# Optimization experiments

Measured on AMD Instinct MI355X. Metric: run time of the kernel, lower is better.

The kernel has to match this reference:

```python
import jax, jax.numpy as jnp
import numpy as np

V, E = 32000, 256
B, S = 8, 512
NA, NC, NS = 12, 24, 576  # N_AXIOMS, N_COMPOSITES, N_STATE
DECAY = 0.9
EPS = 1e-5


def _xavier(key, shape):
    fan_in, fan_out = shape[0], shape[1]
    lim = np.sqrt(6.0 / (fan_in + fan_out))
    return jax.random.uniform(key, shape, jnp.float32, -lim, lim)


def setup_inputs() -> dict:
    key = jax.random.key(0)
    ks = jax.random.split(key, 8)
    return {
        "input_ids": jax.random.randint(ks[0], (B, S), 0, V),
        "embed_table": 0.02 * jax.random.normal(ks[1], (V, E), jnp.float32),
        "ax_w": _xavier(ks[2], (E, NA)), "ax_b": jnp.zeros((NA,), jnp.float32),
        "ax_g": jnp.ones((NA,), jnp.float32), "ax_beta": jnp.zeros((NA,), jnp.float32),
        "comp_w": _xavier(ks[3], (NA, NC)), "comp_b": jnp.zeros((NC,), jnp.float32),
        "comp_g": jnp.ones((NC,), jnp.float32), "comp_beta": jnp.zeros((NC,), jnp.float32),
        "mix": jnp.asarray(0.1, jnp.float32),
        "out_w1": _xavier(ks[4], (NS, 512)), "out_b1": jnp.zeros((512,), jnp.float32),
        "out_w2": _xavier(ks[5], (512, V)), "out_b2": jnp.zeros((V,), jnp.float32),
    }


def _ln(x, g, b):
    m = jnp.mean(x, axis=-1, keepdims=True)
    v = jnp.var(x, axis=-1, keepdims=True)
    return (x - m) * jax.lax.rsqrt(v + EPS) * g + b


def reference(input_ids, embed_table, ax_w, ax_b, ax_g, ax_beta,
              comp_w, comp_b, comp_g, comp_beta, mix,
              out_w1, out_b1, out_w2, out_b2):
    # Embedding lookup (dropout is identity at eval)
    embeds = embed_table[input_ids]                              # [B,S,E]
    # The axiom/composite branches have no time dependence -> compute all steps at once
    axioms = jnp.tanh(_ln(embeds @ ax_w + ax_b, ax_g, ax_beta))  # [B,S,12]
    comps = jnp.tanh(_ln(axioms @ comp_w + comp_b, comp_g, comp_beta))  # [B,S,24]

    sig_mix = jax.nn.sigmoid(mix)
    state0 = jnp.zeros((input_ids.shape[0], NC, NC), jnp.float32)

    def step(state, c):  # c: [B,24]
        state = DECAY * state + sig_mix * (c[:, :, None] * c[:, None, :])
        h = jax.nn.gelu(state.reshape(state.shape[0], NS) @ out_w1 + out_b1,
                        approximate=False)
        logits = h @ out_w2 + out_b2                             # [B,V]
        return state, logits

    final_state, logits = jax.lax.scan(step, state0, jnp.swapaxes(comps, 0, 1))
    return jnp.swapaxes(logits, 0, 1), final_state               # [B,S,V], [B,24,24]
```

## Files before the change

kernel.cpp:

```cpp
#include <hip/hip_runtime.h>
#include <hip/hip_bf16.h>
#include <math.h>

#define BB 8
#define SS 512
#define VV 32000
#define EE 256
#define NAx 12
#define NCc 24
#define NSt 576
#define MM (BB*SS)

typedef __bf16 bf16x8 __attribute__((ext_vector_type(8)));
typedef float f32x4 __attribute__((ext_vector_type(4)));

#define MFMA16(a, b, c) __builtin_amdgcn_mfma_f32_16x16x32_bf16((a), (b), (c), 0, 0, 0)

__device__ __forceinline__ void gl2lds16(const void* g, void* l) {
  __builtin_amdgcn_global_load_lds(
      (const __attribute__((address_space(1))) void*)g,
      (__attribute__((address_space(3))) void*)l, 16, 0, 0);
}

#define FENCE() asm volatile("" ::: "memory")
#define BAR()   do { FENCE(); __builtin_amdgcn_s_barrier(); FENCE(); } while (0)

__global__ __launch_bounds__(256) void k_transpose64(
    const float* __restrict__ in, __hip_bfloat16* __restrict__ out, int R, int C)
{
  __shared__ float t[64][65];
  const int tx = threadIdx.x, ty = threadIdx.y;
  const int c0 = blockIdx.x * 64, r0 = blockIdx.y * 64;
#pragma unroll
  for (int i = 0; i < 64; i += 4)
    t[ty + i][tx] = in[(size_t)(r0 + ty + i) * C + (c0 + tx)];
  __syncthreads();
#pragma unroll
  for (int i = 0; i < 64; i += 4)
    out[(size_t)(c0 + ty + i) * R + (r0 + tx)] = __float2bfloat16(t[tx][ty + i]);
}

__global__ __launch_bounds__(64) void k_embed_comps(
    const int* __restrict__ ids, const float* __restrict__ ET,
    const float* __restrict__ axw, const float* __restrict__ axb,
    const float* __restrict__ axg, const float* __restrict__ axbeta,
    const float* __restrict__ cw,  const float* __restrict__ cb,
    const float* __restrict__ cg,  const float* __restrict__ cbeta,
    float* __restrict__ comps)
{
  __shared__ float sw[EE * NAx];
  __shared__ float scw[NAx * NCc];
  const int tid = threadIdx.x;
  for (int i = tid; i < EE * NAx; i += 64) sw[i] = axw[i];
  for (int i = tid; i < NAx * NCc; i += 64) scw[i] = cw[i];
  __syncthreads();

  const int m = blockIdx.x * 64 + tid;
  const int id = ids[m];
  const float4* e4 = reinterpret_cast<const float4*>(ET + (size_t)id * EE);

  float a[NAx];
#pragma unroll
  for (int t = 0; t < NAx; ++t) a[t] = axb[t];

  for (int q = 0; q < EE / 4; ++q) {
    float4 v = e4[q];
#pragma unroll
    for (int c = 0; c < 4; ++c) {
      float x = (c == 0) ? v.x : (c == 1) ? v.y : (c == 2) ? v.z : v.w;
      const float* wrow = &sw[(q * 4 + c) * NAx];
#pragma unroll
      for (int t = 0; t < NAx; ++t) a[t] += x * wrow[t];
    }
  }
  {
    float mean = 0.f;
#pragma unroll
    for (int t = 0; t < NAx; ++t) mean += a[t];
    mean *= (1.0f / NAx);
    float var = 0.f;
#pragma unroll
    for (int t = 0; t < NAx; ++t) { float d = a[t] - mean; var += d * d; }
    var *= (1.0f / NAx);
    float rs = rsqrtf(var + 1e-5f);
#pragma unroll
    for (int t = 0; t < NAx; ++t)
      a[t] = tanhf((a[t] - mean) * rs * axg[t] + axbeta[t]);
  }
  float c24[NCc];
#pragma unroll
  for (int j = 0; j < NCc; ++j) c24[j] = cb[j];
#pragma unroll
  for (int t = 0; t < NAx; ++t) {
    float x = a[t];
    const float* wrow = &scw[t * NCc];
#pragma unroll
    for (int j = 0; j < NCc; ++j) c24[j] += x * wrow[j];
  }
  {
    float mean = 0.f;
#pragma unroll
    for (int j = 0; j < NCc; ++j) mean += c24[j];
    mean *= (1.0f / NCc);
    float var = 0.f;
#pragma unroll
    for (int j = 0; j < NCc; ++j) { float d = c24[j] - mean; var += d * d; }
    var *= (1.0f / NCc);
    float rs = rsqrtf(var + 1e-5f);
#pragma unroll
    for (int j = 0; j < NCc; ++j)
      c24[j] = tanhf((c24[j] - mean) * rs * cg[j] + cbeta[j]);
  }
#pragma unroll
  for (int j = 0; j < NCc; ++j) comps[(size_t)m * NCc + j] = c24[j];
}

__global__ __launch_bounds__(576) void k_recurrence(
    const float* __restrict__ comps, const float* __restrict__ mix,
    __hip_bfloat16* __restrict__ ST, float* __restrict__ fstate)
{
  __shared__ float sc[SS * NCc];
  const int b = blockIdx.x, tid = threadIdx.x;
  const float* src = comps + (size_t)b * SS * NCc;
  for (int i = tid; i < SS * NCc; i += 576) sc[i] = src[i];
  __syncthreads();

  const float sm = 1.0f / (1.0f + expf(-mix[0]));
  const int i = tid / NCc, j = tid - i * NCc;
  float st = 0.0f;
  __hip_bfloat16* stp = ST + (size_t)b * SS * NSt + tid;
  for (int t = 0; t < SS; ++t) {
    float ci = sc[t * NCc + i], cj = sc[t * NCc + j];
    st = 0.9f * st + sm * ci * cj;
    stp[(size_t)t * NSt] = __float2bfloat16(st);
  }
  fstate[b * NSt + tid] = st;
}

__global__ __launch_bounds__(256) void k_gemm_bt_gelu(
    const __hip_bfloat16* __restrict__ A,
    const __hip_bfloat16* __restrict__ Bt,
    const float* __restrict__ bias,
    __hip_bfloat16* __restrict__ Cb,
    int M, int N, int K)
{
  __shared__ __align__(16) __hip_bfloat16 As[128 * 32];
  __shared__ __align__(16) __hip_bfloat16 Bs[128 * 32];
  const int tid  = threadIdx.x;
  const int lane = tid & 63;
  const int w    = tid >> 6;
  const int wr   = w >> 1, wc = w & 1;
  const int m0 = blockIdx.y * 128;
  const int n0 = blockIdx.x * 128;
  const int lr = lane & 15;
  const int kb = lane >> 4;

  f32x4 acc[4][4];
#pragma unroll
  for (int i = 0; i < 4; ++i)
#pragma unroll
    for (int j = 0; j < 4; ++j) acc[i][j] = (f32x4){0.f, 0.f, 0.f, 0.f};

  for (int k0 = 0; k0 < K; k0 += 32) {
    __syncthreads();
#pragma unroll
    for (int p = 0; p < 2; ++p) {
      const int lbase = w * 2048 + p * 1024;
      const int o  = lbase + lane * 16;
      const int r  = o >> 6;
      const int sg = (o >> 4) & 3;
      gl2lds16(A  + (size_t)(m0 + r) * K + k0 + sg * 8, (char*)As + lbase);
      gl2lds16(Bt + (size_t)(n0 + r) * K + k0 + sg * 8, (char*)Bs + lbase);
    }
    asm volatile("s_waitcnt vmcnt(0)" ::: "memory");
    __syncthreads();

    bf16x8 af[4], bv[4];
#pragma unroll
    for (int mr = 0; mr < 4; ++mr)
      af[mr] = *reinterpret_cast<const bf16x8*>(&As[(wr * 64 + mr * 16 + lr) * 32 + kb * 8]);
#pragma unroll
    for (int nr = 0; nr < 4; ++nr)
      bv[nr] = *reinterpret_cast<const bf16x8*>(&Bs[(wc * 64 + nr * 16 + lr) * 32 + kb * 8]);
#pragma unroll
    for (int mr = 0; mr < 4; ++mr)
#pragma unroll
      for (int nr = 0; nr < 4; ++nr)
        acc[mr][nr] = MFMA16(af[mr], bv[nr], acc[mr][nr]);
  }

#pragma unroll
  for (int nr = 0; nr < 4; ++nr) {
    const int col = n0 + wc * 64 + nr * 16 + lr;
    const float bvs = bias[col];
#pragma unroll
    for (int mr = 0; mr < 4; ++mr) {
      const int rbase = m0 + wr * 64 + mr * 16 + kb * 4;
#pragma unroll
      for (int r = 0; r < 4; ++r) {
        float v = acc[mr][nr][r] + bvs;
        v = 0.5f * v * (1.0f + erff(v * 0.70710678118654752f));
        Cb[(size_t)(rbase + r) * N + col] = __float2bfloat16(v);
      }
    }
  }
}

__global__ __launch_bounds__(256, 2) void k_gemm2_128(
    const __hip_bfloat16* __restrict__ A,
    const __hip_bfloat16* __restrict__ Bt,
    const float* __restrict__ bias,
    float* __restrict__ C,
    int M, int N, int K, int tiles_m)
{
  __shared__ __align__(16) char smem[65536];

  const int NK  = K >> 6;
  const int tid = threadIdx.x;
  const int lane = tid & 63;
  const int w  = tid >> 6;
  const int wr = w >> 1;
  const int wc = w & 1;
  const int lr = lane & 15;
  const int kb = lane >> 4;

  const int nwg = gridDim.x;
  const int cpx = nwg >> 3;
  const int s   = ((int)blockIdx.x & 7) * cpx + ((int)blockIdx.x >> 3);
  const int nt  = s / tiles_m;
  const int mt  = s - nt * tiles_m;
  const int m0  = mt << 7;
  const int n0  = nt << 7;

  const int srow = tid >> 3;
  const int scol = ((tid & 7) ^ (srow & 7)) << 3;
  const int swz0 = (kb ^ (lr & 7)) << 4;
  const int swz1 = swz0 ^ 64;

#define STAGE_A(buf, R, tk0)                                              \
  gl2lds16(A + (size_t)(m0 + (R) + srow) * K + (tk0) + scol,              \
           smem + (buf)*16384 + (R)*128 + w*1024)
#define STAGE_B(buf, R, tk0)                                              \
  gl2lds16(Bt + (size_t)(n0 + (R) + srow) * K + (tk0) + scol,             \
           smem + 32768 + (buf)*16384 + (R)*128 + w*1024)

#define LDA(buf, mf, kh) \
  (*(const bf16x8*)(smem + (buf)*16384 + (wr*64 + (mf)*16 + lr)*128 + ((kh) ? swz1 : swz0)))
#define LDB(buf, nf, kh) \
  (*(const bf16x8*)(smem + 32768 + (buf)*16384 + (wc*64 + (nf)*16 + lr)*128 + ((kh) ? swz1 : swz0)))

  f32x4 acc[4][4];
#pragma unroll
  for (int i = 0; i < 4; ++i)
#pragma unroll
    for (int j = 0; j < 4; ++j) acc[i][j] = (f32x4){0.f, 0.f, 0.f, 0.f};

  float bvs[4];
#pragma unroll
  for (int nf = 0; nf < 4; ++nf) bvs[nf] = bias[n0 + wc * 64 + nf * 16 + lr];

  STAGE_A(0, 0, 0);  STAGE_A(0, 32, 0);  STAGE_A(0, 64, 0);  STAGE_A(0, 96, 0);
  STAGE_B(0, 0, 0);  STAGE_B(0, 32, 0);  STAGE_B(0, 64, 0);  STAGE_B(0, 96, 0);
  STAGE_B(1, 0, 64); STAGE_B(1, 32, 64); STAGE_B(1, 64, 64); STAGE_B(1, 96, 64);
  asm volatile("s_waitcnt vmcnt(4)" ::: "memory");
  BAR();

#pragma unroll 1
  for (int t = 0; t < NK; ++t) {
    const int c  = t & 1;
    const int k1 = (t + 1) << 6;
    const int k2 = (t + 2) << 6;
    bf16x8 a0[4], b0[4], a1[4], b1[4];

#pragma unroll
    for (int mf = 0; mf < 4; ++mf) a0[mf] = LDA(c, mf, 0);
#pragma unroll
    for (int nf = 0; nf < 4; ++nf) b0[nf] = LDB(c, nf, 0);
    if (t < NK - 1) { STAGE_A(c ^ 1, 0, k1); STAGE_A(c ^ 1, 32, k1); }
    BAR();
    asm volatile("s_waitcnt lgkmcnt(0)" ::: "memory");
    __builtin_amdgcn_sched_barrier(0);
    __builtin_amdgcn_s_setprio(1);
#pragma unroll
    for (int mf = 0; mf < 4; ++mf) {
      acc[mf][0] = MFMA16(a0[mf], b0[0], acc[mf][0]);
      acc[mf][1] = MFMA16(a0[mf], b0[1], acc[mf][1]);
    }
    __builtin_amdgcn_s_setprio(0);
    BAR();

#pragma unroll
    for (int mf = 0; mf < 4; ++mf) a1[mf] = LDA(c, mf, 1);
#pragma unroll
    for (int nf = 0; nf < 4; ++nf) b1[nf] = LDB(c, nf, 1);
    if (t < NK - 1) { STAGE_A(c ^ 1, 64, k1); STAGE_A(c ^ 1, 96, k1); }
    BAR();
    asm volatile("s_waitcnt lgkmcnt(0)" ::: "memory");
    __builtin_amdgcn_sched_barrier(0);
    __builtin_amdgcn_s_setprio(1);
#pragma unroll
    for (int mf = 0; mf < 4; ++mf) {
      acc[mf][2] = MFMA16(a0[mf], b0[2], acc[mf][2]);
      acc[mf][3] = MFMA16(a0[mf], b0[3], acc[mf][3]);
    }
    __builtin_amdgcn_s_setprio(0);
    BAR();

    if (t < NK - 2) { STAGE_B(c, 0, k2); STAGE_B(c, 32, k2); }
    BAR();
    __builtin_amdgcn_s_setprio(1);
#pragma unroll
    for (int mf = 0; mf < 4; ++mf) {
      acc[mf][0] = MFMA16(a1[mf], b1[0], acc[mf][0]);
      acc[mf][1] = MFMA16(a1[mf], b1[1], acc[mf][1]);
    }
    __builtin_amdgcn_s_setprio(0);
    BAR();

    if (t < NK - 2) { STAGE_B(c, 64, k2); STAGE_B(c, 96, k2); }
    BAR();
    __builtin_amdgcn_s_setprio(1);
#pragma unroll
    for (int mf = 0; mf < 4; ++mf) {
      acc[mf][2] = MFMA16(a1[mf], b1[2], acc[mf][2]);
      acc[mf][3] = MFMA16(a1[mf], b1[3], acc[mf][3]);
    }
    __builtin_amdgcn_s_setprio(0);
    if (t < NK - 2) {
      asm volatile("s_waitcnt vmcnt(4)" ::: "memory");
    } else if (t == NK - 2) {
      asm volatile("s_waitcnt vmcnt(0)" ::: "memory");
    }
    BAR();
  }

  float* ls = (float*)smem;
#pragma unroll
  for (int mf = 0; mf < 4; ++mf) {
#pragma unroll
    for (int nf = 0; nf < 4; ++nf) {
      const int col = wc * 64 + nf * 16 + lr;
#pragma unroll
      for (int r = 0; r < 4; ++r) {
        const int row = wr * 64 + mf * 16 + kb * 4 + r;
        const int seg = (col >> 2) ^ (row & 7);
        ls[row * 128 + seg * 4 + (col & 3)] = acc[mf][nf][r] + bvs[nf];
      }
    }
  }
  asm volatile("s_waitcnt lgkmcnt(0)" ::: "memory");
  BAR();
#pragma unroll
  for (int pass = 0; pass < 16; ++pass) {
    const int lrow = pass * 8 + w * 2 + (lane >> 5);
    const int seg  = (lane & 31) ^ (lrow & 7);
    f32x4 v = *(const f32x4*)&ls[lrow * 128 + seg * 4];
    __builtin_nontemporal_store(v,
        (f32x4*)&C[(size_t)(m0 + lrow) * N + n0 + (lane & 31) * 4]);
  }
#undef STAGE_A
#undef STAGE_B
#undef LDA
#undef LDB
}

extern "C" void kernel_launch(void* const* d_in, const int* in_sizes, int n_in,
                              void* d_out, int out_size, void* d_ws, size_t ws_size,
                              hipStream_t stream) {
  const int*   ids  = (const int*)  d_in[0];
  const float* ET   = (const float*)d_in[1];
  const float* axw  = (const float*)d_in[2];
  const float* axb  = (const float*)d_in[3];
  const float* axg  = (const float*)d_in[4];
  const float* axbt = (const float*)d_in[5];
  const float* cw   = (const float*)d_in[6];
  const float* cb   = (const float*)d_in[7];
  const float* cg   = (const float*)d_in[8];
  const float* cbt  = (const float*)d_in[9];
  const float* mix  = (const float*)d_in[10];
  const float* w1   = (const float*)d_in[11];
  const float* b1   = (const float*)d_in[12];
  const float* w2   = (const float*)d_in[13];
  const float* b2   = (const float*)d_in[14];

  float* out = (float*)d_out;

  char* ws = (char*)d_ws;
  size_t o = 0;
  __hip_bfloat16* W2T   = (__hip_bfloat16*)(ws + o); o += (size_t)VV * 512 * 2;
  __hip_bfloat16* W1T   = (__hip_bfloat16*)(ws + o); o += (size_t)512 * NSt * 2;
  float*          comps = (float*)(ws + o);          o += (size_t)MM * NCc * 4;
  __hip_bfloat16* STb   = (__hip_bfloat16*)(ws + o); o += (size_t)MM * NSt * 2;
  __hip_bfloat16* H     = (__hip_bfloat16*)(ws + o); o += (size_t)MM * 512 * 2;

  k_transpose64<<<dim3(VV / 64, 512 / 64), dim3(64, 4), 0, stream>>>(w2, W2T, 512, VV);
  k_transpose64<<<dim3(512 / 64, NSt / 64), dim3(64, 4), 0, stream>>>(w1, W1T, NSt, 512);

  k_embed_comps<<<MM / 64, 64, 0, stream>>>(ids, ET, axw, axb, axg, axbt,
                                            cw, cb, cg, cbt, comps);

  k_recurrence<<<BB, NSt, 0, stream>>>(comps, mix, STb, out + (size_t)MM * VV);

  k_gemm_bt_gelu<<<dim3(512 / 128, MM / 128), 256, 0, stream>>>(
      STb, W1T, b1, H, MM, 512, NSt);

  k_gemm2_128<<<(VV / 128) * (MM / 128), 256, 0, stream>>>(
      H, W2T, b2, out, MM, VV, 512, MM / 128);
}
```

Measured before the change: 273.4 us.

## Restructure output GEMM to 128x256 tiles with BK=32 double buffering

Rewrites the big logits GEMM to use 128x256 output tiles, with each wave computing 64x128, and a K-step of 32 instead of 64. The A and B tiles are staged two steps ahead in a simpler single-phase loop with fewer barriers. The LDS-transposed coalesced epilogue is replaced by direct scalar nontemporal stores. Wider tiles raise arithmetic intensity and cut A reloads. The costs are double the accumulator registers, which may hurt occupancy under launch_bounds(256,2), and uncoalesced scalar stores of a very large fp32 output.

```diff
diff --git a/kernel.cpp b/kernel.cpp
--- a/kernel.cpp
+++ b/kernel.cpp
@@ -206,16 +206,16 @@
   }
 }
 
-__global__ __launch_bounds__(256, 2) void k_gemm2_128(
+__global__ __launch_bounds__(256, 2) void k_gemm2_bk32(
     const __hip_bfloat16* __restrict__ A,
     const __hip_bfloat16* __restrict__ Bt,
     const float* __restrict__ bias,
     float* __restrict__ C,
     int M, int N, int K, int tiles_m)
 {
-  __shared__ __align__(16) char smem[65536];
-
-  const int NK  = K >> 6;
+  __shared__ __align__(16) char smem[49152];
+
+  const int NK  = K >> 5;
   const int tid = threadIdx.x;
   const int lane = tid & 63;
   const int w  = tid >> 6;
@@ -230,133 +230,95 @@
   const int nt  = s / tiles_m;
   const int mt  = s - nt * tiles_m;
   const int m0  = mt << 7;
-  const int n0  = nt << 7;
-
-  const int srow = tid >> 3;
-  const int scol = ((tid & 7) ^ (srow & 7)) << 3;
-  const int swz0 = (kb ^ (lr & 7)) << 4;
-  const int swz1 = swz0 ^ 64;
-
-#define STAGE_A(buf, R, tk0)                                              \
-  gl2lds16(A + (size_t)(m0 + (R) + srow) * K + (tk0) + scol,              \
-           smem + (buf)*16384 + (R)*128 + w*1024)
-#define STAGE_B(buf, R, tk0)                                              \
-  gl2lds16(Bt + (size_t)(n0 + (R) + srow) * K + (tk0) + scol,             \
-           smem + 32768 + (buf)*16384 + (R)*128 + w*1024)
-
-#define LDA(buf, mf, kh) \
-  (*(const bf16x8*)(smem + (buf)*16384 + (wr*64 + (mf)*16 + lr)*128 + ((kh) ? swz1 : swz0)))
-#define LDB(buf, nf, kh) \
-  (*(const bf16x8*)(smem + 32768 + (buf)*16384 + (wc*64 + (nf)*16 + lr)*128 + ((kh) ? swz1 : swz0)))
-
-  f32x4 acc[4][4];
+  const int n0  = nt << 8;
+
+  const int scol = (((lane & 3) ^ ((lane >> 3) & 3)) << 3);
+  const int rsw  = ((kb ^ ((lr >> 1) & 3)) << 4);
+
+#define STAGE_A(buf, j, tk0)                                               \
+  gl2lds16(A + (size_t)(m0 + w*32 + (j)*16 + (lane >> 2)) * K + (tk0) + scol, \
+           smem + (buf)*8192 + w*2048 + (j)*1024 + lane*16)
+#define STAGE_B(buf, j, tk0)                                               \
+  gl2lds16(Bt + (size_t)(n0 + w*64 + (j)*16 + (lane >> 2)) * K + (tk0) + scol, \
+           smem + 16384 + (buf)*16384 + w*4096 + (j)*1024 + lane*16)
+
+#define LDA(buf, mf) \
+  (*(const bf16x8*)(smem + (buf)*8192 + (wr*64 + (mf)*16 + lr)*64 + rsw))
+#define LDB(buf, nf) \
+  (*(const bf16x8*)(smem + 16384 + (buf)*16384 + (wc*128 + (nf)*16 + lr)*64 + rsw))
+
+  f32x4 acc[4][8];
 #pragma unroll
   for (int i = 0; i < 4; ++i)
 #pragma unroll
-    for (int j = 0; j < 4; ++j) acc[i][j] = (f32x4){0.f, 0.f, 0.f, 0.f};
-
-  float bvs[4];
-#pragma unroll
-  for (int nf = 0; nf < 4; ++nf) bvs[nf] = bias[n0 + wc * 64 + nf * 16 + lr];
-
-  STAGE_A(0, 0, 0);  STAGE_A(0, 32, 0);  STAGE_A(0, 64, 0);  STAGE_A(0, 96, 0);
-  STAGE_B(0, 0, 0);  STAGE_B(0, 32, 0);  STAGE_B(0, 64, 0);  STAGE_B(0, 96, 0);
-  STAGE_B(1, 0, 64); STAGE_B(1, 32, 64); STAGE_B(1, 64, 64); STAGE_B(1, 96, 64);
-  asm volatile("s_waitcnt vmcnt(4)" ::: "memory");
+    for (int j = 0; j < 8; ++j) acc[i][j] = (f32x4){0.f, 0.f, 0.f, 0.f};
+
+  float bvs[8];
+#pragma unroll
+  for (int nf = 0; nf < 8; ++nf) bvs[nf] = bias[n0 + wc * 128 + nf * 16 + lr];
+
+  STAGE_A(0, 0, 0);  STAGE_A(0, 1, 0);
+  STAGE_B(0, 0, 0);  STAGE_B(0, 1, 0);  STAGE_B(0, 2, 0);  STAGE_B(0, 3, 0);
+  STAGE_A(1, 0, 32); STAGE_A(1, 1, 32);
+  STAGE_B(1, 0, 32); STAGE_B(1, 1, 32); STAGE_B(1, 2, 32); STAGE_B(1, 3, 32);
+  asm volatile("s_waitcnt vmcnt(6)" ::: "memory");
   BAR();
 
 #pragma unroll 1
   for (int t = 0; t < NK; ++t) {
     const int c  = t & 1;
-    const int k1 = (t + 1) << 6;
-    const int k2 = (t + 2) << 6;
-    bf16x8 a0[4], b0[4], a1[4], b1[4];
-
-#pragma unroll
-    for (int mf = 0; mf < 4; ++mf) a0[mf] = LDA(c, mf, 0);
-#pragma unroll
-    for (int nf = 0; nf < 4; ++nf) b0[nf] = LDB(c, nf, 0);
-    if (t < NK - 1) { STAGE_A(c ^ 1, 0, k1); STAGE_A(c ^ 1, 32, k1); }
-    BAR();
+    const int k2 = (t + 2) << 5;
+    bf16x8 a[4], b[8];
+
+#pragma unroll
+    for (int mf = 0; mf < 4; ++mf) a[mf] = LDA(c, mf);
+#pragma unroll
+    for (int nf = 0; nf < 8; ++nf) b[nf] = LDB(c, nf);
     asm volatile("s_waitcnt lgkmcnt(0)" ::: "memory");
     __builtin_amdgcn_sched_barrier(0);
     __builtin_amdgcn_s_setprio(1);
 #pragma unroll
     for (int mf = 0; mf < 4; ++mf) {
-      acc[mf][0] = MFMA16(a0[mf], b0[0], acc[mf][0]);
-      acc[mf][1] = MFMA16(a0[mf], b0[1], acc[mf][1]);
+      acc[mf][0] = MFMA16(a[mf], b[0], acc[mf][0]);
+      acc[mf][1] = MFMA16(a[mf], b[1], acc[mf][1]);
+      acc[mf][2] = MFMA16(a[mf], b[2], acc[mf][2]);
+      acc[mf][3] = MFMA16(a[mf], b[3], acc[mf][3]);
     }
     __builtin_amdgcn_s_setprio(0);
     BAR();
 
-#pragma unroll
-    for (int mf = 0; mf < 4; ++mf) a1[mf] = LDA(c, mf, 1);
-#pragma unroll
-    for (int nf = 0; nf < 4; ++nf) b1[nf] = LDB(c, nf, 1);
-    if (t < NK - 1) { STAGE_A(c ^ 1, 64, k1); STAGE_A(c ^ 1, 96, k1); }
-    BAR();
-    asm volatile("s_waitcnt lgkmcnt(0)" ::: "memory");
-    __builtin_amdgcn_sched_barrier(0);
+    if (t < NK - 2) {
+      STAGE_A(c, 0, k2); STAGE_A(c, 1, k2);
+      STAGE_B(c, 0, k2); STAGE_B(c, 1, k2); STAGE_B(c, 2, k2); STAGE_B(c, 3, k2);
+    }
     __builtin_amdgcn_s_setprio(1);
 #pragma unroll
     for (int mf = 0; mf < 4; ++mf) {
-      acc[mf][2] = MFMA16(a0[mf], b0[2], acc[mf][2]);
-      acc[mf][3] = MFMA16(a0[mf], b0[3], acc[mf][3]);
-    }
-    __builtin_amdgcn_s_setprio(0);
-    BAR();
-
-    if (t < NK - 2) { STAGE_B(c, 0, k2); STAGE_B(c, 32, k2); }
-    BAR();
-    __builtin_amdgcn_s_setprio(1);
-#pragma unroll
-    for (int mf = 0; mf < 4; ++mf) {
-      acc[mf][0] = MFMA16(a1[mf], b1[0], acc[mf][0]);
-      acc[mf][1] = MFMA16(a1[mf], b1[1], acc[mf][1]);
-    }
-    __builtin_amdgcn_s_setprio(0);
-    BAR();
-
-    if (t < NK - 2) { STAGE_B(c, 64, k2); STAGE_B(c, 96, k2); }
-    BAR();
-    __builtin_amdgcn_s_setprio(1);
-#pragma unroll
-    for (int mf = 0; mf < 4; ++mf) {
-      acc[mf][2] = MFMA16(a1[mf], b1[2], acc[mf][2]);
-      acc[mf][3] = MFMA16(a1[mf], b1[3], acc[mf][3]);
+      acc[mf][4] = MFMA16(a[mf], b[4], acc[mf][4]);
+      acc[mf][5] = MFMA16(a[mf], b[5], acc[mf][5]);
+      acc[mf][6] = MFMA16(a[mf], b[6], acc[mf][6]);
+      acc[mf][7] = MFMA16(a[mf], b[7], acc[mf][7]);
     }
     __builtin_amdgcn_s_setprio(0);
     if (t < NK - 2) {
-      asm volatile("s_waitcnt vmcnt(4)" ::: "memory");
+      asm volatile("s_waitcnt vmcnt(6)" ::: "memory");
     } else if (t == NK - 2) {
       asm volatile("s_waitcnt vmcnt(0)" ::: "memory");
     }
     BAR();
   }
 
-  float* ls = (float*)smem;
-#pragma unroll
-  for (int mf = 0; mf < 4; ++mf) {
-#pragma unroll
-    for (int nf = 0; nf < 4; ++nf) {
-      const int col = wc * 64 + nf * 16 + lr;
-#pragma unroll
-      for (int r = 0; r < 4; ++r) {
-        const int row = wr * 64 + mf * 16 + kb * 4 + r;
-        const int seg = (col >> 2) ^ (row & 7);
-        ls[row * 128 + seg * 4 + (col & 3)] = acc[mf][nf][r] + bvs[nf];
-      }
-    }
-  }
-  asm volatile("s_waitcnt lgkmcnt(0)" ::: "memory");
-  BAR();
-#pragma unroll
-  for (int pass = 0; pass < 16; ++pass) {
-    const int lrow = pass * 8 + w * 2 + (lane >> 5);
-    const int seg  = (lane & 31) ^ (lrow & 7);
-    f32x4 v = *(const f32x4*)&ls[lrow * 128 + seg * 4];
-    __builtin_nontemporal_store(v,
-        (f32x4*)&C[(size_t)(m0 + lrow) * N + n0 + (lane & 31) * 4]);
+#pragma unroll
+  for (int nf = 0; nf < 8; ++nf) {
+    const int col = n0 + wc * 128 + nf * 16 + lr;
+#pragma unroll
+    for (int mf = 0; mf < 4; ++mf) {
+      const int rbase = m0 + wr * 64 + mf * 16 + kb * 4;
+#pragma unroll
+      for (int r = 0; r < 4; ++r)
+        __builtin_nontemporal_store(acc[mf][nf][r] + bvs[nf],
+                                    &C[(size_t)(rbase + r) * N + col]);
+    }
   }
 #undef STAGE_A
 #undef STAGE_B
@@ -404,6 +366,6 @@
   k_gemm_bt_gelu<<<dim3(512 / 128, MM / 128), 256, 0, stream>>>(
       STb, W1T, b1, H, MM, 512, NSt);
 
-  k_gemm2_128<<<(VV / 128) * (MM / 128), 256, 0, stream>>>(
+  k_gemm2_bk32<<<(MM / 128) * (VV / 256), 256, 0, stream>>>(
       H, W2T, b2, out, MM, VV, 512, MM / 128);
 }
```

After: 285.2 us. +4.3%, slower.
